# Kernel tuning notes

Hardware: AMD Instinct MI355X
Metric: run time of the kernel (lower is better)

The kernel has to match this reference:

```python
import jax, jax.numpy as jnp
import numpy as np

T = 8192
N = 2048
SPECTRAL_RADIUS = 0.9
WASHOUT = 200


def setup_inputs() -> dict:
    key = jax.random.key(0)
    ku, kin, kres = jax.random.split(key, 3)
    u = jax.random.normal(ku, (T,), dtype=jnp.float32)
    W_in = jax.random.normal(kin, (N,), dtype=jnp.float32)
    W_res = np.asarray(jax.random.normal(kres, (N, N), dtype=jnp.float32))
    # __init__: rescale reservoir to target spectral radius
    spec_rad = float(np.max(np.abs(np.linalg.eigvals(W_res.astype(np.float64)))))
    if spec_rad != 0:
        W_res = W_res * (SPECTRAL_RADIUS / spec_rad)
    return {
        "u": u,
        "W_in": W_in,
        "W_res": jnp.asarray(W_res, dtype=jnp.float32),
        "washout": WASHOUT,
    }


def reference(u, W_in, W_res, washout):
    # Sequential ESN recurrence: x_t = tanh(W_in * u_t + W_res @ x_{t-1})
    n = W_res.shape[0]

    def step(x, u_t):
        x_new = jnp.tanh(W_in * u_t + W_res @ x)  # [N]
        return x_new, x_new

    x0 = jnp.zeros((n,), dtype=W_res.dtype)
    _, X = jax.lax.scan(step, x0, u)  # X: [T, N]
    return X[washout:]  # states after washout (fed to the readout)
```

## Files before the change

kernel.cpp:

```cpp
#include <hip/hip_runtime.h>

#define TSTEPS 8192
#define NDIM   2048
#define NBLK   128
#define NTHR   512
#define RPB    16

typedef float f32x4 __attribute__((ext_vector_type(4)));
typedef int   i32x4 __attribute__((ext_vector_type(4)));
typedef float f32x2 __attribute__((ext_vector_type(2)));

__device__ __forceinline__ unsigned ld_u32_agent(const unsigned* p) {
  return __hip_atomic_load((unsigned*)p, __ATOMIC_RELAXED, __HIP_MEMORY_SCOPE_AGENT);
}
__device__ __forceinline__ void st_u32_agent(unsigned* p, unsigned v) {
  __hip_atomic_store(p, v, __ATOMIC_RELAXED, __HIP_MEMORY_SCOPE_AGENT);
}
__device__ __forceinline__ void ld_2x4_agent(const i32x4* p0, const i32x4* p1,
                                             i32x4& r0, i32x4& r1) {
  asm volatile("global_load_dwordx4 %0, %2, off sc1\n\t"
               "global_load_dwordx4 %1, %3, off sc1\n\t"
               "s_waitcnt vmcnt(0)"
               : "=&v"(r0), "=&v"(r1) : "v"(p0), "v"(p1) : "memory");
}
__device__ __forceinline__ void st_x4_agent(f32x4* p, f32x4 v) {
  asm volatile("global_store_dwordx4 %0, %1, off sc1" :: "v"(p), "v"(v) : "memory");
}

__global__ void __launch_bounds__(NTHR, 1) esn_persistent(
    const float* __restrict__ u,
    const float* __restrict__ W_in,
    const float* __restrict__ W_res,
    const int* __restrict__ washout_p,
    float* __restrict__ out,
    unsigned* __restrict__ ws)
{
  const int tid  = threadIdx.x;
  const int bid  = blockIdx.x;
  const int wave = tid >> 6;
  const int lane = tid & 63;
  const int row0 = bid * RPB + wave * 2;
  const int washout = washout_p[0];

  unsigned* abortw = ws + 144;
  float* pair0 = (float*)((char*)ws + 1024);
  float* pair1 = pair0 + 2 * NDIM;

  __shared__ __align__(16) float x_lds[NDIM];
  __shared__ __align__(16) float xpair_lds[2 * RPB];
  __shared__ __align__(16) float xval_lds[RPB];
  __shared__ int s_abort;
  if (tid == 0) s_abort = 0;

  const f32x4* Wr0 = (const f32x4*)(W_res + (size_t)row0 * NDIM) + lane;
  const f32x4* Wr1 = (const f32x4*)(W_res + (size_t)(row0 + 1) * NDIM) + lane;
  const f32x4 w00 = Wr0[0 * 64], w01 = Wr0[1 * 64], w02 = Wr0[2 * 64], w03 = Wr0[3 * 64];
  const f32x4 w04 = Wr0[4 * 64], w05 = Wr0[5 * 64], w06 = Wr0[6 * 64], w07 = Wr0[7 * 64];
  const f32x4 w10 = Wr1[0 * 64], w11 = Wr1[1 * 64], w12 = Wr1[2 * 64], w13 = Wr1[3 * 64];
  const f32x4 w14 = Wr1[4 * 64], w15 = Wr1[5 * 64], w16 = Wr1[6 * 64], w17 = Wr1[7 * 64];
  const float win0 = W_in[row0];
  const float win1 = W_in[row0 + 1];

  for (int t = 0; t < TSTEPS; ++t) {
    const i32x4* src = (const i32x4*)((t & 1) ? pair1 : pair0);
    const int want = t;
    i32x4 r0, r1;
    bool ok;
    {
      unsigned g = 0;
      do {
        ld_2x4_agent(src + tid, src + NTHR + tid, r0, r1);
        ok = (r0.y == want) & (r0.w == want) & (r1.y == want) & (r1.w == want);
        if (!ok && ((++g & 255u) == 0u)) {
          if (ld_u32_agent(abortw) != 0u) break;
          if (g > (1u << 20)) { st_u32_agent(abortw, 1u); break; }
        }
      } while (!ok);
    }
    if (!ok) s_abort = 1;
    {
      f32x2 v01, v23;
      v01.x = __int_as_float(r0.x); v01.y = __int_as_float(r0.z);
      v23.x = __int_as_float(r1.x); v23.y = __int_as_float(r1.z);
      ((f32x2*)x_lds)[tid]        = v01;
      ((f32x2*)x_lds)[NTHR + tid] = v23;
    }
    const float ut = u[t];
    __syncthreads();
    if (s_abort) return;

    float a0 = 0.f, b0 = 0.f, a1 = 0.f, b1 = 0.f;
    const f32x4* x4v = (const f32x4*)x_lds + lane;
#define ESN_DOT(WA, WB, K, A, B) { const f32x4 xv = x4v[(K) * 64];            \
      A += WA.x * xv.x; A += WA.y * xv.y; A += WA.z * xv.z; A += WA.w * xv.w; \
      B += WB.x * xv.x; B += WB.y * xv.y; B += WB.z * xv.z; B += WB.w * xv.w; }
    ESN_DOT(w00, w10, 0, a0, a1) ESN_DOT(w01, w11, 1, b0, b1)
    ESN_DOT(w02, w12, 2, a0, a1) ESN_DOT(w03, w13, 3, b0, b1)
    ESN_DOT(w04, w14, 4, a0, a1) ESN_DOT(w05, w15, 5, b0, b1)
    ESN_DOT(w06, w16, 6, a0, a1) ESN_DOT(w07, w17, 7, b0, b1)
#undef ESN_DOT
    const float s0 = a0 + b0;
    const float s1 = a1 + b1;
    const float c0 = s0 + __shfl_xor(s0, 32, 64);
    const float c1 = s1 + __shfl_xor(s1, 32, 64);
    float c = (lane < 32) ? c0 : c1;
#pragma unroll
    for (int off = 16; off > 0; off >>= 1) c += __shfl_xor(c, off, 64);

    if ((lane & 31) == 0) {
      const float wi  = (lane == 0) ? win0 : win1;
      const float pre = wi * ut + c;
      const float e2  = __expf(2.0f * pre);
      const float th  = 1.0f - __fdividef(2.0f, e2 + 1.0f);
      const int   i   = wave * 2 + (lane >> 5);
      xval_lds[i] = th;
      ((f32x2*)xpair_lds)[i] = (f32x2){ th, __int_as_float(t + 1) };
    }
    __syncthreads();

    if (tid < 12) {
      if (tid < 8) {
        f32x4* dst = (f32x4*)(((t + 1) & 1) ? pair1 : pair0) + bid * 8 + tid;
        st_x4_agent(dst, ((const f32x4*)xpair_lds)[tid]);
      } else if (t >= washout) {
        float4* orow = (float4*)(out + (size_t)(t - washout) * NDIM) + bid * 4 + (tid - 8);
        const f32x4 vv = ((const f32x4*)xval_lds)[tid - 8];
        float4 v; v.x = vv.x; v.y = vv.y; v.z = vv.z; v.w = vv.w;
        *orow = v;
      }
    }
  }
}

extern "C" void kernel_launch(void* const* d_in, const int* in_sizes, int n_in,
                              void* d_out, int out_size, void* d_ws, size_t ws_size,
                              hipStream_t stream) {
  const float* u       = (const float*)d_in[0];
  const float* W_in    = (const float*)d_in[1];
  const float* W_res   = (const float*)d_in[2];
  const int*   washout = (const int*)d_in[3];
  float*       out     = (float*)d_out;

  (void)hipMemsetAsync(d_ws, 0, 1024 + 4 * 2 * NDIM * 2, stream);

  esn_persistent<<<dim3(NBLK), dim3(NTHR), 0, stream>>>(
      u, W_in, W_res, washout, out, (unsigned*)d_ws);
}
```

Baseline: 18.20 ms.

## Pack broadcast state as bf16 value plus 16-bit step tag per word

```diff
diff --git a/kernel.cpp b/kernel.cpp
--- a/kernel.cpp
+++ b/kernel.cpp
@@ -6,9 +6,8 @@
 #define NTHR   512
 #define RPB    16
 
-typedef float f32x4 __attribute__((ext_vector_type(4)));
-typedef int   i32x4 __attribute__((ext_vector_type(4)));
-typedef float f32x2 __attribute__((ext_vector_type(2)));
+typedef float    f32x4 __attribute__((ext_vector_type(4)));
+typedef unsigned u32x4 __attribute__((ext_vector_type(4)));
 
 __device__ __forceinline__ unsigned ld_u32_agent(const unsigned* p) {
   return __hip_atomic_load((unsigned*)p, __ATOMIC_RELAXED, __HIP_MEMORY_SCOPE_AGENT);
@@ -16,15 +15,20 @@
 __device__ __forceinline__ void st_u32_agent(unsigned* p, unsigned v) {
   __hip_atomic_store(p, v, __ATOMIC_RELAXED, __HIP_MEMORY_SCOPE_AGENT);
 }
-__device__ __forceinline__ void ld_2x4_agent(const i32x4* p0, const i32x4* p1,
-                                             i32x4& r0, i32x4& r1) {
-  asm volatile("global_load_dwordx4 %0, %2, off sc1\n\t"
-               "global_load_dwordx4 %1, %3, off sc1\n\t"
-               "s_waitcnt vmcnt(0)"
-               : "=&v"(r0), "=&v"(r1) : "v"(p0), "v"(p1) : "memory");
+__device__ __forceinline__ u32x4 ld_x4_agent(const u32x4* p) {
+  u32x4 r;
+  asm volatile("global_load_dwordx4 %0, %1, off sc1\n\ts_waitcnt vmcnt(0)"
+               : "=v"(r) : "v"(p) : "memory");
+  return r;
 }
-__device__ __forceinline__ void st_x4_agent(f32x4* p, f32x4 v) {
+__device__ __forceinline__ void st_x4_agent(u32x4* p, u32x4 v) {
   asm volatile("global_store_dwordx4 %0, %1, off sc1" :: "v"(p), "v"(v) : "memory");
+}
+__device__ __forceinline__ f32x4 ld_w_sync(const f32x4* p) {
+  f32x4 r;
+  asm volatile("global_load_dwordx4 %0, %1, off\n\ts_waitcnt vmcnt(0)"
+               : "=v"(r) : "v"(p));
+  return r;
 }
 
 __global__ void __launch_bounds__(NTHR, 1) esn_persistent(
@@ -43,34 +47,39 @@
   const int washout = washout_p[0];
 
   unsigned* abortw = ws + 144;
-  float* pair0 = (float*)((char*)ws + 1024);
-  float* pair1 = pair0 + 2 * NDIM;
+  unsigned* buf0   = ws + 256;
+  unsigned* buf1   = buf0 + NDIM;
 
-  __shared__ __align__(16) float x_lds[NDIM];
-  __shared__ __align__(16) float xpair_lds[2 * RPB];
-  __shared__ __align__(16) float xval_lds[RPB];
+  __shared__ __align__(16) float    x_lds[NDIM];
+  __shared__ __align__(16) unsigned xpack_lds[RPB];
+  __shared__ __align__(16) float    xval_lds[RPB];
   __shared__ int s_abort;
   if (tid == 0) s_abort = 0;
 
   const f32x4* Wr0 = (const f32x4*)(W_res + (size_t)row0 * NDIM) + lane;
   const f32x4* Wr1 = (const f32x4*)(W_res + (size_t)(row0 + 1) * NDIM) + lane;
-  const f32x4 w00 = Wr0[0 * 64], w01 = Wr0[1 * 64], w02 = Wr0[2 * 64], w03 = Wr0[3 * 64];
-  const f32x4 w04 = Wr0[4 * 64], w05 = Wr0[5 * 64], w06 = Wr0[6 * 64], w07 = Wr0[7 * 64];
-  const f32x4 w10 = Wr1[0 * 64], w11 = Wr1[1 * 64], w12 = Wr1[2 * 64], w13 = Wr1[3 * 64];
-  const f32x4 w14 = Wr1[4 * 64], w15 = Wr1[5 * 64], w16 = Wr1[6 * 64], w17 = Wr1[7 * 64];
+  const f32x4 w00 = ld_w_sync(Wr0 + 0 * 64), w01 = ld_w_sync(Wr0 + 1 * 64);
+  const f32x4 w02 = ld_w_sync(Wr0 + 2 * 64), w03 = ld_w_sync(Wr0 + 3 * 64);
+  const f32x4 w04 = ld_w_sync(Wr0 + 4 * 64), w05 = ld_w_sync(Wr0 + 5 * 64);
+  const f32x4 w06 = ld_w_sync(Wr0 + 6 * 64), w07 = ld_w_sync(Wr0 + 7 * 64);
+  const f32x4 w10 = ld_w_sync(Wr1 + 0 * 64), w11 = ld_w_sync(Wr1 + 1 * 64);
+  const f32x4 w12 = ld_w_sync(Wr1 + 2 * 64), w13 = ld_w_sync(Wr1 + 3 * 64);
+  const f32x4 w14 = ld_w_sync(Wr1 + 4 * 64), w15 = ld_w_sync(Wr1 + 5 * 64);
+  const f32x4 w16 = ld_w_sync(Wr1 + 6 * 64), w17 = ld_w_sync(Wr1 + 7 * 64);
   const float win0 = W_in[row0];
   const float win1 = W_in[row0 + 1];
 
   for (int t = 0; t < TSTEPS; ++t) {
-    const i32x4* src = (const i32x4*)((t & 1) ? pair1 : pair0);
-    const int want = t;
-    i32x4 r0, r1;
+    const u32x4* src = (const u32x4*)((t & 1) ? buf1 : buf0) + tid;
+    const unsigned want = (unsigned)t;
+    u32x4 r;
     bool ok;
     {
       unsigned g = 0;
       do {
-        ld_2x4_agent(src + tid, src + NTHR + tid, r0, r1);
-        ok = (r0.y == want) & (r0.w == want) & (r1.y == want) & (r1.w == want);
+        r = ld_x4_agent(src);
+        ok = ((((r.x ^ want) | (r.y ^ want)) |
+               ((r.z ^ want) | (r.w ^ want))) & 0xFFFFu) == 0u;
         if (!ok && ((++g & 255u) == 0u)) {
           if (ld_u32_agent(abortw) != 0u) break;
           if (g > (1u << 20)) { st_u32_agent(abortw, 1u); break; }
@@ -79,11 +88,12 @@
     }
     if (!ok) s_abort = 1;
     {
-      f32x2 v01, v23;
-      v01.x = __int_as_float(r0.x); v01.y = __int_as_float(r0.z);
-      v23.x = __int_as_float(r1.x); v23.y = __int_as_float(r1.z);
-      ((f32x2*)x_lds)[tid]        = v01;
-      ((f32x2*)x_lds)[NTHR + tid] = v23;
+      f32x4 xv;
+      xv.x = __uint_as_float(r.x & 0xFFFF0000u);
+      xv.y = __uint_as_float(r.y & 0xFFFF0000u);
+      xv.z = __uint_as_float(r.z & 0xFFFF0000u);
+      xv.w = __uint_as_float(r.w & 0xFFFF0000u);
+      ((f32x4*)x_lds)[tid] = xv;
     }
     const float ut = u[t];
     __syncthreads();
@@ -114,17 +124,19 @@
       const float th  = 1.0f - __fdividef(2.0f, e2 + 1.0f);
       const int   i   = wave * 2 + (lane >> 5);
       xval_lds[i] = th;
-      ((f32x2*)xpair_lds)[i] = (f32x2){ th, __int_as_float(t + 1) };
+      const unsigned b  = __float_as_uint(th);
+      const unsigned bf = (b + 0x7fffu + ((b >> 16) & 1u)) & 0xFFFF0000u;
+      xpack_lds[i] = bf | (unsigned)(t + 1);
     }
     __syncthreads();
 
-    if (tid < 12) {
-      if (tid < 8) {
-        f32x4* dst = (f32x4*)(((t + 1) & 1) ? pair1 : pair0) + bid * 8 + tid;
-        st_x4_agent(dst, ((const f32x4*)xpair_lds)[tid]);
+    if (tid < 8) {
+      if (tid < 4) {
+        u32x4* dst = (u32x4*)(((t + 1) & 1) ? buf1 : buf0) + bid * 4 + tid;
+        st_x4_agent(dst, ((const u32x4*)xpack_lds)[tid]);
       } else if (t >= washout) {
-        float4* orow = (float4*)(out + (size_t)(t - washout) * NDIM) + bid * 4 + (tid - 8);
-        const f32x4 vv = ((const f32x4*)xval_lds)[tid - 8];
+        float4* orow = (float4*)(out + (size_t)(t - washout) * NDIM) + bid * 4 + (tid - 4);
+        const f32x4 vv = ((const f32x4*)xval_lds)[tid - 4];
         float4 v; v.x = vv.x; v.y = vv.y; v.z = vv.z; v.w = vv.w;
         *orow = v;
       }
@@ -141,7 +153,7 @@
   const int*   washout = (const int*)d_in[3];
   float*       out     = (float*)d_out;
 
-  (void)hipMemsetAsync(d_ws, 0, 1024 + 4 * 2 * NDIM * 2, stream);
+  (void)hipMemsetAsync(d_ws, 0, 1024 + 2 * NDIM * 4, stream);
 
   esn_persistent<<<dim3(NBLK), dim3(NTHR), 0, stream>>>(
       u, W_in, W_res, washout, out, (unsigned*)d_ws);
```

New measurement: 18.24 ms. About the same (+0.2%).
